# Kernel tuning notes

Hardware: AMD Instinct MI355X
Metric: run time of the kernel (lower is better)

The kernel has to match this reference:

```python
import jax, jax.numpy as jnp
import numpy as np

N, T, D, H = 64, 1024, 1024, 1024


def setup_inputs() -> dict:
    key = jax.random.key(0)
    k1, k2, k3, k4 = jax.random.split(key, 4)
    x = jax.random.normal(k1, (N, T, D), dtype=jnp.float32)
    h0 = jax.random.normal(k2, (N, H), dtype=jnp.float32)
    Wx = jax.random.normal(k3, (D, 4 * H), dtype=jnp.float32) / np.sqrt(D)
    Wh = jax.random.normal(k4, (H, 4 * H), dtype=jnp.float32) / np.sqrt(H)
    b = jnp.zeros((4 * H,), dtype=jnp.float32)
    return {"x": x, "h0": h0, "Wx": Wx, "Wh": Wh, "b": b}


def reference(x, h0, Wx, Wh, b):
    # x: [N, T, D], h0: [N, H] -> hn: [N, T, H]
    Hd = h0.shape[1]
    c0 = jnp.zeros_like(h0)
    # Precompute input contribution for all timesteps in one big GEMM:
    # identical math to per-step x_t @ Wx, far fewer launches.
    xW = jnp.einsum("ntd,dg->ntg", x, Wx) + b  # [N, T, 4H]

    def step(carry, xw_t):
        prev_h, prev_c = carry
        preact = xw_t + prev_h @ Wh  # [N, 4H]
        ai, af, ao, ag = jnp.split(preact, 4, axis=1)
        i = jax.nn.sigmoid(ai)
        f = jax.nn.sigmoid(af)
        o = jax.nn.sigmoid(ao)
        g = jnp.tanh(ag)
        next_c = f * prev_c + i * g
        next_h = o * jnp.tanh(next_c)
        return (next_h, next_c), next_h

    xW_t = jnp.swapaxes(xW, 0, 1)  # [T, N, 4H] for scan over time
    _, hs = jax.lax.scan(step, (h0, c0), xW_t)
    return jnp.swapaxes(hs, 0, 1)  # [N, T, H]
```

## Files before the change

### kernel.cpp

```cpp
#include <hip/hip_runtime.h>

typedef unsigned short u16;
typedef unsigned long long u64;
typedef __attribute__((ext_vector_type(8))) short short8;
typedef __attribute__((ext_vector_type(4))) float f32x4;

#define DEVINL __device__ __forceinline__

constexpr int Nb = 64;
constexpr int Tt = 1024;
constexpr int Dd = 1024;
constexpr int Hh = 1024;
constexpr int NWG = 256;
constexpr int TPB = 256;
constexpr int TWG = 128;
constexpr int MS  = 32;

DEVINL u16 f2b(float f) {
  union { float f; unsigned u; } v; v.f = f;
  unsigned r = (v.u + 0x7fffu + ((v.u >> 16) & 1u)) >> 16;
  return (u16)r;
}
DEVINL float sigm(float x) { return 1.f / (1.f + __expf(-x)); }
DEVINL float tanhfast(float x) { float e = __expf(2.f * x); return 1.f - 2.f / (e + 1.f); }

DEVINL short8 ldh16(const u16* p) {
  u64 a = __hip_atomic_load((const u64*)p,       __ATOMIC_RELAXED, __HIP_MEMORY_SCOPE_AGENT);
  u64 b = __hip_atomic_load((const u64*)(p + 4), __ATOMIC_RELAXED, __HIP_MEMORY_SCOPE_AGENT);
  union { u64 q[2]; short8 v; } u;
  u.q[0] = a; u.q[1] = b;
  return u.v;
}

DEVINL void bar_w() {
  asm volatile("s_waitcnt lgkmcnt(0)" ::: "memory");
  __builtin_amdgcn_s_barrier();
}

__global__ void cvt_x_kernel(const float* __restrict__ x, u16* __restrict__ xb) {
  size_t i = ((size_t)blockIdx.x * TPB + threadIdx.x) * 8;
  float4 a = *reinterpret_cast<const float4*>(x + i);
  float4 b = *reinterpret_cast<const float4*>(x + i + 4);
  short8 r;
  r[0] = (short)f2b(a.x); r[1] = (short)f2b(a.y);
  r[2] = (short)f2b(a.z); r[3] = (short)f2b(a.w);
  r[4] = (short)f2b(b.x); r[5] = (short)f2b(b.y);
  r[6] = (short)f2b(b.z); r[7] = (short)f2b(b.w);
  *reinterpret_cast<short8*>(xb + i) = r;
}

template<bool XBF16, bool HIST>
__global__ __launch_bounds__(TPB, 1) void lstm_team(
    const float* __restrict__ x, const u16* __restrict__ xb,
    const float* __restrict__ h0, const float* __restrict__ Wx,
    const float* __restrict__ Wh, const float* __restrict__ bias,
    float* __restrict__ out, u16* __restrict__ hmem,
    unsigned* __restrict__ flg)
{
  __shared__ u16 Bt[32][2048];
  __shared__ float ex[4][32][36];
  __shared__ unsigned pubcnt;

  const int g   = blockIdx.x;
  const int tid = threadIdx.x;
  const int w   = tid >> 6;
  const int l   = tid & 63;

  const int team = ((g & 7) < 4) ? 0 : 1;
  const int r    = (g >> 3) * 4 + (g & 3);
  const int n0   = team * MS;
  const int jc0  = r * 8;

  unsigned* tFlg = flg + team * TWG;
  u16* hb0 = HIST ? hmem + (size_t)team * ((size_t)Tt * MS * Hh)
                  : hmem + (size_t)team * (2 * MS * Hh);

  if (tid == 0) pubcnt = 0u;

  for (int idx = tid; idx < 32 * 2048; idx += TPB) {
    int k = idx >> 5;
    int c = idx & 31;
    int pc = (c >> 3) * 1024 + jc0 + (c & 7);
    float v = (k < 1024) ? Wh[(size_t)k * 4096 + pc]
                         : Wx[(size_t)(k - 1024) * 4096 + pc];
    Bt[c][k ^ ((c & 7) << 3)] = f2b(v);
  }

  if (tid < 64) {
    int n  = tid >> 1;
    int jc = (tid & 1) * 4;
    const float* hp = h0 + (size_t)(n0 + n) * Hh + jc0 + jc;
    u64 pk = (u64)f2b(hp[0]) | ((u64)f2b(hp[1]) << 16) |
             ((u64)f2b(hp[2]) << 32) | ((u64)f2b(hp[3]) << 48);
    __hip_atomic_store((u64*)(hb0 + n * Hh + jc0 + jc), pk,
                       __ATOMIC_RELAXED, __HIP_MEMORY_SCOPE_AGENT);
    asm volatile("s_waitcnt vmcnt(0)" ::: "memory");
    if (tid == 0)
      __hip_atomic_store(&tFlg[r], 1u, __ATOMIC_RELAXED, __HIP_MEMORY_SCOPE_AGENT);
  }
  __syncthreads();

  const int jj = tid & 7;
  const int nE = tid >> 3;
  const float bI = bias[0 * 1024 + jc0 + jj];
  const float bF = bias[1 * 1024 + jc0 + jj];
  const float bO = bias[2 * 1024 + jc0 + jj];
  const float bG = bias[3 * 1024 + jc0 + jj];
  float c_reg = 0.f;

  const int arow = l & 15;
  const int kg   = (l >> 4) * 8;
  const int kb   = w * 256;
  const int sw   = (l & 7) << 3;
  const u16* bp0 = &Bt[l & 15][0];
  const u16* bp1 = &Bt[16 | (l & 15)][0];

  short8 bh0[8], bh1[8], bx0[8], bx1[8];
  #pragma unroll
  for (int i = 0; i < 8; ++i) {
    int ka = (kb + kg + 32 * i) ^ sw;
    bh0[i] = *reinterpret_cast<const short8*>(bp0 + ka);
    bh1[i] = *reinterpret_cast<const short8*>(bp1 + ka);
    int kx = (1024 + kb + kg + 32 * i) ^ sw;
    bx0[i] = *reinterpret_cast<const short8*>(bp0 + kx);
    bx1[i] = *reinterpret_cast<const short8*>(bp1 + kx);
  }

  for (int t = 0; t < Tt; ++t) {
    const u16* hb  = HIST ? hb0 + (size_t)t * (MS * Hh)
                          : hb0 + (t & 1) * (MS * Hh);
    u16*       hbn = HIST ? hb0 + (size_t)(t + 1) * (MS * Hh)
                          : hb0 + ((t + 1) & 1) * (MS * Hh);

    short8 xv0[8], xv1[8];
    if constexpr (XBF16) {
      const u16* xr0 = xb + ((size_t)(n0 + arow)      * Tt + t) * Dd + kb + kg;
      const u16* xr1 = xb + ((size_t)(n0 + 16 + arow) * Tt + t) * Dd + kb + kg;
      #pragma unroll
      for (int i = 0; i < 8; ++i) {
        xv0[i] = *reinterpret_cast<const short8*>(xr0 + 32 * i);
        xv1[i] = *reinterpret_cast<const short8*>(xr1 + 32 * i);
      }
    } else {
      const float* xr0 = x + ((size_t)(n0 + arow)      * Tt + t) * Dd + kb + kg;
      const float* xr1 = x + ((size_t)(n0 + 16 + arow) * Tt + t) * Dd + kb + kg;
      #pragma unroll
      for (int i = 0; i < 8; ++i) {
        float4 a0 = *reinterpret_cast<const float4*>(xr0 + 32 * i);
        float4 a1 = *reinterpret_cast<const float4*>(xr0 + 32 * i + 4);
        float4 c0 = *reinterpret_cast<const float4*>(xr1 + 32 * i);
        float4 c1 = *reinterpret_cast<const float4*>(xr1 + 32 * i + 4);
        short8 v0, v1;
        v0[0]=(short)f2b(a0.x); v0[1]=(short)f2b(a0.y);
        v0[2]=(short)f2b(a0.z); v0[3]=(short)f2b(a0.w);
        v0[4]=(short)f2b(a1.x); v0[5]=(short)f2b(a1.y);
        v0[6]=(short)f2b(a1.z); v0[7]=(short)f2b(a1.w);
        v1[0]=(short)f2b(c0.x); v1[1]=(short)f2b(c0.y);
        v1[2]=(short)f2b(c0.z); v1[3]=(short)f2b(c0.w);
        v1[4]=(short)f2b(c1.x); v1[5]=(short)f2b(c1.y);
        v1[6]=(short)f2b(c1.z); v1[7]=(short)f2b(c1.w);
        xv0[i] = v0; xv1[i] = v1;
      }
    }

    f32x4 a00 = {0.f,0.f,0.f,0.f}, a01 = {0.f,0.f,0.f,0.f};
    f32x4 a10 = {0.f,0.f,0.f,0.f}, a11 = {0.f,0.f,0.f,0.f};

    #pragma unroll
    for (int i = 0; i < 8; ++i) {
      a00 = __builtin_amdgcn_mfma_f32_16x16x32_bf16(xv0[i], bx0[i], a00, 0, 0, 0);
      a01 = __builtin_amdgcn_mfma_f32_16x16x32_bf16(xv0[i], bx1[i], a01, 0, 0, 0);
      a10 = __builtin_amdgcn_mfma_f32_16x16x32_bf16(xv1[i], bx0[i], a10, 0, 0, 0);
      a11 = __builtin_amdgcn_mfma_f32_16x16x32_bf16(xv1[i], bx1[i], a11, 0, 0, 0);
    }

    {
      const unsigned ep = (unsigned)(t + 1);
      bool rdy;
      do {
        unsigned f = 0xFFFFFFFFu;
        if (l < 32)
          f = __hip_atomic_load(&tFlg[32 * w + l], __ATOMIC_RELAXED,
                                __HIP_MEMORY_SCOPE_AGENT);
        rdy = (bool)__all(f >= ep);
        if (!rdy) __builtin_amdgcn_s_sleep(1);
      } while (!rdy);
    }
    while (__hip_atomic_load(&pubcnt, __ATOMIC_RELAXED,
                             __HIP_MEMORY_SCOPE_WORKGROUP) < (unsigned)(4 * t))
      __builtin_amdgcn_s_sleep(1);
    asm volatile("" ::: "memory");

    short8 hv0[8], hv1[8];
    {
      const u16* hr = hb + (size_t)arow * Hh + kb + kg;
      #pragma unroll
      for (int i = 0; i < 8; ++i) {
        if constexpr (HIST) {
          hv0[i] = *reinterpret_cast<const short8*>(hr + 32 * i);
          hv1[i] = *reinterpret_cast<const short8*>(hr + 16 * Hh + 32 * i);
        } else {
          hv0[i] = ldh16(hr + 32 * i);
          hv1[i] = ldh16(hr + 16 * Hh + 32 * i);
        }
      }
    }

    #pragma unroll
    for (int i = 0; i < 8; ++i) {
      a00 = __builtin_amdgcn_mfma_f32_16x16x32_bf16(hv0[i], bh0[i], a00, 0, 0, 0);
      a01 = __builtin_amdgcn_mfma_f32_16x16x32_bf16(hv0[i], bh1[i], a01, 0, 0, 0);
      a10 = __builtin_amdgcn_mfma_f32_16x16x32_bf16(hv1[i], bh0[i], a10, 0, 0, 0);
      a11 = __builtin_amdgcn_mfma_f32_16x16x32_bf16(hv1[i], bh1[i], a11, 0, 0, 0);
    }

    #pragma unroll
    for (int q = 0; q < 4; ++q) {
      ex[w][ 0 + (l >> 4) * 4 + q][ 0 + (l & 15)] = a00[q];
      ex[w][ 0 + (l >> 4) * 4 + q][16 + (l & 15)] = a01[q];
      ex[w][16 + (l >> 4) * 4 + q][ 0 + (l & 15)] = a10[q];
      ex[w][16 + (l >> 4) * 4 + q][16 + (l & 15)] = a11[q];
    }
    bar_w();

    float pI = bI, pF = bF, pO = bO, pG = bG;
    #pragma unroll
    for (int wv = 0; wv < 4; ++wv) {
      pI += ex[wv][nE][ 0 + jj];
      pF += ex[wv][nE][ 8 + jj];
      pO += ex[wv][nE][16 + jj];
      pG += ex[wv][nE][24 + jj];
    }
    const float ig = sigm(pI), fg = sigm(pF), og = sigm(pO);
    const float gg = tanhfast(pG);
    c_reg = fg * c_reg + ig * gg;
    const float hv = og * tanhfast(c_reg);

    {
      int hb16 = (int)f2b(hv);
      int pb   = __shfl_xor(hb16, 1, 64);
      if ((tid & 1) == 0) {
        unsigned pk = (unsigned)(hb16 & 0xFFFF) | ((unsigned)(pb & 0xFFFF) << 16);
        __hip_atomic_store((unsigned*)(hbn + nE * Hh + jc0 + jj), pk,
                           __ATOMIC_RELAXED, __HIP_MEMORY_SCOPE_AGENT);
      }
      asm volatile("s_waitcnt vmcnt(0)" ::: "memory");
      if (l == 0) {
        unsigned old = __hip_atomic_fetch_add(&pubcnt, 1u, __ATOMIC_RELAXED,
                                              __HIP_MEMORY_SCOPE_WORKGROUP);
        if (old == (unsigned)(4 * t + 3) && t + 1 < Tt)
          __hip_atomic_store(&tFlg[r], (unsigned)(t + 2),
                             __ATOMIC_RELAXED, __HIP_MEMORY_SCOPE_AGENT);
      }
    }

    out[((size_t)(n0 + nE) * Tt + t) * Hh + jc0 + jj] = hv;
  }
}

extern "C" void kernel_launch(void* const* d_in, const int* in_sizes, int n_in,
                              void* d_out, int out_size, void* d_ws, size_t ws_size,
                              hipStream_t stream) {
  const float* x    = (const float*)d_in[0];
  const float* h0   = (const float*)d_in[1];
  const float* Wx   = (const float*)d_in[2];
  const float* Wh   = (const float*)d_in[3];
  const float* bias = (const float*)d_in[4];
  float* out = (float*)d_out;

  char* wsb = (char*)d_ws;
  unsigned* flg = (unsigned*)wsb;

  const size_t hist_off   = (size_t)1 << 20;
  const size_t hist_bytes = (size_t)2 * Tt * MS * Hh * 2;
  const size_t xb_bytes   = (size_t)Nb * Tt * Dd * 2;

  const bool use_hist = ws_size >= hist_off + hist_bytes;
  const size_t xb_off = use_hist ? hist_off + hist_bytes : hist_off;
  const bool use_xb   = ws_size >= xb_off + xb_bytes;

  u16* hmem = use_hist ? (u16*)(wsb + hist_off) : (u16*)(wsb + 65536);
  u16* xb   = (u16*)(wsb + xb_off);

  hipMemsetAsync(wsb, 0, 40960, stream);

  void* args[] = {(void*)&x, (void*)&xb, (void*)&h0, (void*)&Wx, (void*)&Wh,
                  (void*)&bias, (void*)&out, (void*)&hmem, (void*)&flg};
  if (use_xb)
    cvt_x_kernel<<<dim3((Nb * Tt * Dd) / (8 * TPB)), dim3(TPB), 0, stream>>>(x, xb);

  const void* kfn =
      use_hist ? (use_xb ? (const void*)lstm_team<true, true>
                         : (const void*)lstm_team<false, true>)
               : (use_xb ? (const void*)lstm_team<true, false>
                         : (const void*)lstm_team<false, false>);
  hipLaunchCooperativeKernel(kfn, dim3(NWG), dim3(TPB), args, 0, stream);
}
```

Baseline: 5.635 ms.

## Precompute input projection with a separate bf16 MFMA GEMM before recurrent kernel

Adds a transposed bf16 conversion of Wx and a tiled, double-buffered MFMA GEMM that computes x@Wx for all timesteps into workspace, in fp32 or bf16 depending on workspace size. The persistent LSTM kernel then loads the precomputed gate preactivations instead of running the x-side MFMAs each step, which shortens the serial per-step critical path. In exchange it writes and reads a large intermediate (up to 1 GiB fp32) and runs extra kernels. It falls back to the old fused path when workspace is too small.

```diff
diff --git a/kernel.cpp b/kernel.cpp
--- a/kernel.cpp
+++ b/kernel.cpp
@@ -20,6 +20,10 @@
   union { float f; unsigned u; } v; v.f = f;
   unsigned r = (v.u + 0x7fffu + ((v.u >> 16) & 1u)) >> 16;
   return (u16)r;
+}
+DEVINL float b2f(u16 b) {
+  union { unsigned u; float f; } v; v.u = ((unsigned)b) << 16;
+  return v.f;
 }
 DEVINL float sigm(float x) { return 1.f / (1.f + __expf(-x)); }
 DEVINL float tanhfast(float x) { float e = __expf(2.f * x); return 1.f - 2.f / (e + 1.f); }
@@ -49,13 +53,105 @@
   *reinterpret_cast<short8*>(xb + i) = r;
 }
 
-template<bool XBF16, bool HIST>
+__global__ void cvt_wt_kernel(const float* __restrict__ wx, u16* __restrict__ wxt) {
+  int gid = blockIdx.x * TPB + threadIdx.x;
+  int k  = gid >> 9;
+  int nb = (gid & 511) * 8;
+  const float* p = wx + (size_t)k * 4096 + nb;
+  #pragma unroll
+  for (int i = 0; i < 8; ++i)
+    wxt[(size_t)(nb + i) * 1024 + k] = f2b(p[i]);
+}
+
+template<bool F32OUT>
+__global__ __launch_bounds__(TPB) void gemm_xw(
+    const u16* __restrict__ A, const u16* __restrict__ B, void* __restrict__ C)
+{
+  __shared__ u16 Al[2][128][40];
+  __shared__ u16 Bl[2][128][40];
+  const int tid = threadIdx.x;
+  const int w = tid >> 6, l = tid & 63;
+  const int mt = blockIdx.x >> 5, nt = blockIdx.x & 31;
+  const size_t m0 = (size_t)mt * 128, n0 = (size_t)nt * 128;
+  const int wr = w >> 1, wc = w & 1;
+  const int srow = tid >> 2;
+  const int scol = (tid & 3) * 8;
+  const int arow = l & 15, kg = (l >> 4) * 8;
+
+  f32x4 acc[4][4];
+  #pragma unroll
+  for (int i = 0; i < 4; ++i)
+    #pragma unroll
+    for (int j = 0; j < 4; ++j) acc[i][j] = (f32x4){0.f, 0.f, 0.f, 0.f};
+
+  #pragma unroll
+  for (int rr = 0; rr < 2; ++rr) {
+    int row = rr * 64 + srow;
+    short8 sa = *reinterpret_cast<const short8*>(A + (m0 + row) * 1024 + scol);
+    short8 sb = *reinterpret_cast<const short8*>(B + (n0 + row) * 1024 + scol);
+    *reinterpret_cast<short8*>(&Al[0][row][scol]) = sa;
+    *reinterpret_cast<short8*>(&Bl[0][row][scol]) = sb;
+  }
+  bar_w();
+
+  int cur = 0;
+  for (int ks = 0; ks < 32; ++ks) {
+    short8 na[2], nb2[2];
+    if (ks < 31) {
+      #pragma unroll
+      for (int rr = 0; rr < 2; ++rr) {
+        int row = rr * 64 + srow;
+        na[rr]  = *reinterpret_cast<const short8*>(A + (m0 + row) * 1024 + (ks + 1) * 32 + scol);
+        nb2[rr] = *reinterpret_cast<const short8*>(B + (n0 + row) * 1024 + (ks + 1) * 32 + scol);
+      }
+    }
+    short8 av[4], bv[4];
+    #pragma unroll
+    for (int tr = 0; tr < 4; ++tr)
+      av[tr] = *reinterpret_cast<const short8*>(&Al[cur][wr * 64 + tr * 16 + arow][kg]);
+    #pragma unroll
+    for (int tc = 0; tc < 4; ++tc)
+      bv[tc] = *reinterpret_cast<const short8*>(&Bl[cur][wc * 64 + tc * 16 + arow][kg]);
+    #pragma unroll
+    for (int tr = 0; tr < 4; ++tr)
+      #pragma unroll
+      for (int tc = 0; tc < 4; ++tc)
+        acc[tr][tc] = __builtin_amdgcn_mfma_f32_16x16x32_bf16(av[tr], bv[tc], acc[tr][tc], 0, 0, 0);
+    if (ks < 31) {
+      #pragma unroll
+      for (int rr = 0; rr < 2; ++rr) {
+        int row = rr * 64 + srow;
+        *reinterpret_cast<short8*>(&Al[cur ^ 1][row][scol]) = na[rr];
+        *reinterpret_cast<short8*>(&Bl[cur ^ 1][row][scol]) = nb2[rr];
+      }
+    }
+    bar_w();
+    cur ^= 1;
+  }
+
+  #pragma unroll
+  for (int tr = 0; tr < 4; ++tr) {
+    int mrow = wr * 64 + tr * 16 + 4 * (l >> 4);
+    #pragma unroll
+    for (int tc = 0; tc < 4; ++tc) {
+      int ncol = wc * 64 + tc * 16 + (l & 15);
+      #pragma unroll
+      for (int q = 0; q < 4; ++q) {
+        size_t off = (m0 + mrow + q) * 4096 + n0 + ncol;
+        if constexpr (F32OUT) ((float*)C)[off] = acc[tr][tc][q];
+        else                  ((u16*)C)[off]   = f2b(acc[tr][tc][q]);
+      }
+    }
+  }
+}
+
+template<int MODE, bool XBF16, bool HIST>
 __global__ __launch_bounds__(TPB, 1) void lstm_team(
     const float* __restrict__ x, const u16* __restrict__ xb,
     const float* __restrict__ h0, const float* __restrict__ Wx,
     const float* __restrict__ Wh, const float* __restrict__ bias,
     float* __restrict__ out, u16* __restrict__ hmem,
-    unsigned* __restrict__ flg)
+    unsigned* __restrict__ flg, const void* __restrict__ xw)
 {
   __shared__ u16 Bt[32][2048];
   __shared__ float ex[4][32][36];
@@ -77,12 +173,16 @@
 
   if (tid == 0) pubcnt = 0u;
 
-  for (int idx = tid; idx < 32 * 2048; idx += TPB) {
-    int k = idx >> 5;
+  constexpr int KW = (MODE == 0) ? 2048 : 1024;
+  for (int idx = tid; idx < 32 * KW; idx += TPB) {
+    int k = idx / 32;
     int c = idx & 31;
     int pc = (c >> 3) * 1024 + jc0 + (c & 7);
-    float v = (k < 1024) ? Wh[(size_t)k * 4096 + pc]
-                         : Wx[(size_t)(k - 1024) * 4096 + pc];
+    float v;
+    if constexpr (MODE == 0)
+      v = (k < 1024) ? Wh[(size_t)k * 4096 + pc] : Wx[(size_t)(k - 1024) * 4096 + pc];
+    else
+      v = Wh[(size_t)k * 4096 + pc];
     Bt[c][k ^ ((c & 7) << 3)] = f2b(v);
   }
 
@@ -121,57 +221,65 @@
     int ka = (kb + kg + 32 * i) ^ sw;
     bh0[i] = *reinterpret_cast<const short8*>(bp0 + ka);
     bh1[i] = *reinterpret_cast<const short8*>(bp1 + ka);
-    int kx = (1024 + kb + kg + 32 * i) ^ sw;
-    bx0[i] = *reinterpret_cast<const short8*>(bp0 + kx);
-    bx1[i] = *reinterpret_cast<const short8*>(bp1 + kx);
+    if constexpr (MODE == 0) {
+      int kx = (1024 + kb + kg + 32 * i) ^ sw;
+      bx0[i] = *reinterpret_cast<const short8*>(bp0 + kx);
+      bx1[i] = *reinterpret_cast<const short8*>(bp1 + kx);
+    }
   }
 
   for (int t = 0; t < Tt; ++t) {
-    const u16* hb  = HIST ? hb0 + (size_t)t * (MS * Hh)
-                          : hb0 + (t & 1) * (MS * Hh);
-    u16*       hbn = HIST ? hb0 + (size_t)(t + 1) * (MS * Hh)
-                          : hb0 + ((t + 1) & 1) * (MS * Hh);
-
-    short8 xv0[8], xv1[8];
-    if constexpr (XBF16) {
-      const u16* xr0 = xb + ((size_t)(n0 + arow)      * Tt + t) * Dd + kb + kg;
-      const u16* xr1 = xb + ((size_t)(n0 + 16 + arow) * Tt + t) * Dd + kb + kg;
-      #pragma unroll
-      for (int i = 0; i < 8; ++i) {
-        xv0[i] = *reinterpret_cast<const short8*>(xr0 + 32 * i);
-        xv1[i] = *reinterpret_cast<const short8*>(xr1 + 32 * i);
-      }
-    } else {
-      const float* xr0 = x + ((size_t)(n0 + arow)      * Tt + t) * Dd + kb + kg;
-      const float* xr1 = x + ((size_t)(n0 + 16 + arow) * Tt + t) * Dd + kb + kg;
-      #pragma unroll
-      for (int i = 0; i < 8; ++i) {
-        float4 a0 = *reinterpret_cast<const float4*>(xr0 + 32 * i);
-        float4 a1 = *reinterpret_cast<const float4*>(xr0 + 32 * i + 4);
-        float4 c0 = *reinterpret_cast<const float4*>(xr1 + 32 * i);
-        float4 c1 = *reinterpret_cast<const float4*>(xr1 + 32 * i + 4);
-        short8 v0, v1;
-        v0[0]=(short)f2b(a0.x); v0[1]=(short)f2b(a0.y);
-        v0[2]=(short)f2b(a0.z); v0[3]=(short)f2b(a0.w);
-        v0[4]=(short)f2b(a1.x); v0[5]=(short)f2b(a1.y);
-        v0[6]=(short)f2b(a1.z); v0[7]=(short)f2b(a1.w);
-        v1[0]=(short)f2b(c0.x); v1[1]=(short)f2b(c0.y);
-        v1[2]=(short)f2b(c0.z); v1[3]=(short)f2b(c0.w);
-        v1[4]=(short)f2b(c1.x); v1[5]=(short)f2b(c1.y);
-        v1[6]=(short)f2b(c1.z); v1[7]=(short)f2b(c1.w);
-        xv0[i] = v0; xv1[i] = v1;
-      }
-    }
+    const u16* hb  = HIST ? hb0 + (size_t)t * (MS * Hh) : hb0 + (t & 1) * (MS * Hh);
+    u16*       hbn = HIST ? hb0 + (size_t)(t + 1) * (MS * Hh) : hb0 + ((t + 1) & 1) * (MS * Hh);
 
     f32x4 a00 = {0.f,0.f,0.f,0.f}, a01 = {0.f,0.f,0.f,0.f};
     f32x4 a10 = {0.f,0.f,0.f,0.f}, a11 = {0.f,0.f,0.f,0.f};
-
-    #pragma unroll
-    for (int i = 0; i < 8; ++i) {
-      a00 = __builtin_amdgcn_mfma_f32_16x16x32_bf16(xv0[i], bx0[i], a00, 0, 0, 0);
-      a01 = __builtin_amdgcn_mfma_f32_16x16x32_bf16(xv0[i], bx1[i], a01, 0, 0, 0);
-      a10 = __builtin_amdgcn_mfma_f32_16x16x32_bf16(xv1[i], bx0[i], a10, 0, 0, 0);
-      a11 = __builtin_amdgcn_mfma_f32_16x16x32_bf16(xv1[i], bx1[i], a11, 0, 0, 0);
+    float xwv0 = 0.f, xwv1 = 0.f, xwv2 = 0.f, xwv3 = 0.f;
+
+    if constexpr (MODE == 0) {
+      short8 xv0[8], xv1[8];
+      if constexpr (XBF16) {
+        const u16* xr0 = xb + ((size_t)(n0 + arow)      * Tt + t) * Dd + kb + kg;
+        const u16* xr1 = xb + ((size_t)(n0 + 16 + arow) * Tt + t) * Dd + kb + kg;
+        #pragma unroll
+        for (int i = 0; i < 8; ++i) {
+          xv0[i] = *reinterpret_cast<const short8*>(xr0 + 32 * i);
+          xv1[i] = *reinterpret_cast<const short8*>(xr1 + 32 * i);
+        }
+      } else {
+        const float* xr0 = x + ((size_t)(n0 + arow)      * Tt + t) * Dd + kb + kg;
+        const float* xr1 = x + ((size_t)(n0 + 16 + arow) * Tt + t) * Dd + kb + kg;
+        #pragma unroll
+        for (int i = 0; i < 8; ++i) {
+          float4 a0 = *reinterpret_cast<const float4*>(xr0 + 32 * i);
+          float4 a1 = *reinterpret_cast<const float4*>(xr0 + 32 * i + 4);
+          float4 c0 = *reinterpret_cast<const float4*>(xr1 + 32 * i);
+          float4 c1 = *reinterpret_cast<const float4*>(xr1 + 32 * i + 4);
+          short8 v0, v1;
+          v0[0]=(short)f2b(a0.x); v0[1]=(short)f2b(a0.y);
+          v0[2]=(short)f2b(a0.z); v0[3]=(short)f2b(a0.w);
+          v0[4]=(short)f2b(a1.x); v0[5]=(short)f2b(a1.y);
+          v0[6]=(short)f2b(a1.z); v0[7]=(short)f2b(a1.w);
+          v1[0]=(short)f2b(c0.x); v1[1]=(short)f2b(c0.y);
+          v1[2]=(short)f2b(c0.z); v1[3]=(short)f2b(c0.w);
+          v1[4]=(short)f2b(c1.x); v1[5]=(short)f2b(c1.y);
+          v1[6]=(short)f2b(c1.z); v1[7]=(short)f2b(c1.w);
+          xv0[i] = v0; xv1[i] = v1;
+        }
+      }
+      #pragma unroll
+      for (int i = 0; i < 8; ++i) {
+        a00 = __builtin_amdgcn_mfma_f32_16x16x32_bf16(xv0[i], bx0[i], a00, 0, 0, 0);
+        a01 = __builtin_amdgcn_mfma_f32_16x16x32_bf16(xv0[i], bx1[i], a01, 0, 0, 0);
+        a10 = __builtin_amdgcn_mfma_f32_16x16x32_bf16(xv1[i], bx0[i], a10, 0, 0, 0);
+        a11 = __builtin_amdgcn_mfma_f32_16x16x32_bf16(xv1[i], bx1[i], a11, 0, 0, 0);
+      }
+    } else if constexpr (MODE == 1) {
+      const float* p = (const float*)xw + ((size_t)(n0 + nE) * Tt + t) * 4096 + jc0 + jj;
+      xwv0 = p[0]; xwv1 = p[1024]; xwv2 = p[2048]; xwv3 = p[3072];
+    } else {
+      const u16* p = (const u16*)xw + ((size_t)(n0 + nE) * Tt + t) * 4096 + jc0 + jj;
+      xwv0 = b2f(p[0]); xwv1 = b2f(p[1024]); xwv2 = b2f(p[2048]); xwv3 = b2f(p[3072]);
     }
 
     {
@@ -223,7 +331,7 @@
     }
     bar_w();
 
-    float pI = bI, pF = bF, pO = bO, pG = bG;
+    float pI = bI + xwv0, pF = bF + xwv1, pO = bO + xwv2, pG = bG + xwv3;
     #pragma unroll
     for (int wv = 0; wv < 4; ++wv) {
       pI += ex[wv][nE][ 0 + jj];
@@ -271,28 +379,60 @@
   char* wsb = (char*)d_ws;
   unsigned* flg = (unsigned*)wsb;
 
-  const size_t hist_off   = (size_t)1 << 20;
-  const size_t hist_bytes = (size_t)2 * Tt * MS * Hh * 2;
-  const size_t xb_bytes   = (size_t)Nb * Tt * Dd * 2;
-
-  const bool use_hist = ws_size >= hist_off + hist_bytes;
-  const size_t xb_off = use_hist ? hist_off + hist_bytes : hist_off;
-  const bool use_xb   = ws_size >= xb_off + xb_bytes;
-
-  u16* hmem = use_hist ? (u16*)(wsb + hist_off) : (u16*)(wsb + 65536);
-  u16* xb   = (u16*)(wsb + xb_off);
+  const size_t off_hist = (size_t)1 << 20;
+  const size_t sz_hist  = (size_t)2 * Tt * MS * Hh * 2;
+  const size_t off_xb   = off_hist + sz_hist;
+  const size_t sz_xb    = (size_t)Nb * Tt * Dd * 2;
+  const size_t off_wt   = off_xb + sz_xb;
+  const size_t sz_wt    = (size_t)4096 * 1024 * 2;
+  const size_t off_xw   = off_wt + sz_wt;
+  const size_t sz_xw32  = (size_t)Nb * Tt * 4096 * 4;
+  const size_t sz_xw16  = sz_xw32 / 2;
+
+  int mode;
+  if      (ws_size >= off_xw + sz_xw32) mode = 1;
+  else if (ws_size >= off_xw + sz_xw16) mode = 2;
+  else                                  mode = 0;
+
+  u16* hmem;
+  u16* xb  = (u16*)(wsb + off_xb);
+  u16* wxt = (u16*)(wsb + off_wt);
+  void* xw = (void*)(wsb + off_xw);
 
   hipMemsetAsync(wsb, 0, 40960, stream);
 
-  void* args[] = {(void*)&x, (void*)&xb, (void*)&h0, (void*)&Wx, (void*)&Wh,
-                  (void*)&bias, (void*)&out, (void*)&hmem, (void*)&flg};
+  if (mode >= 1) {
+    hmem = (u16*)(wsb + off_hist);
+    cvt_x_kernel<<<dim3((Nb * Tt * Dd) / (8 * TPB)), dim3(TPB), 0, stream>>>(x, xb);
+    cvt_wt_kernel<<<dim3(2048), dim3(TPB), 0, stream>>>(Wx, wxt);
+    if (mode == 1)
+      gemm_xw<true><<<dim3(16384), dim3(TPB), 0, stream>>>(xb, wxt, xw);
+    else
+      gemm_xw<false><<<dim3(16384), dim3(TPB), 0, stream>>>(xb, wxt, xw);
+
+    void* args[] = {(void*)&x, (void*)&xb, (void*)&h0, (void*)&Wx, (void*)&Wh,
+                    (void*)&bias, (void*)&out, (void*)&hmem, (void*)&flg, (void*)&xw};
+    const void* kfn = (mode == 1) ? (const void*)lstm_team<1, false, true>
+                                  : (const void*)lstm_team<2, false, true>;
+    hipLaunchCooperativeKernel(kfn, dim3(NWG), dim3(TPB), args, 0, stream);
+    return;
+  }
+
+  const bool use_hist = ws_size >= off_hist + sz_hist;
+  const size_t xb0_off = use_hist ? off_xb : off_hist;
+  const bool use_xb   = ws_size >= xb0_off + sz_xb;
+  hmem = use_hist ? (u16*)(wsb + off_hist) : (u16*)(wsb + 65536);
+  u16* xb0 = (u16*)(wsb + xb0_off);
+
+  void* args[] = {(void*)&x, (void*)&xb0, (void*)&h0, (void*)&Wx, (void*)&Wh,
+                  (void*)&bias, (void*)&out, (void*)&hmem, (void*)&flg, (void*)&xw};
   if (use_xb)
-    cvt_x_kernel<<<dim3((Nb * Tt * Dd) / (8 * TPB)), dim3(TPB), 0, stream>>>(x, xb);
+    cvt_x_kernel<<<dim3((Nb * Tt * Dd) / (8 * TPB)), dim3(TPB), 0, stream>>>(x, xb0);
 
   const void* kfn =
-      use_hist ? (use_xb ? (const void*)lstm_team<true, true>
-                         : (const void*)lstm_team<false, true>)
-               : (use_xb ? (const void*)lstm_team<true, false>
-                         : (const void*)lstm_team<false, false>);
+      use_hist ? (use_xb ? (const void*)lstm_team<0, true,  true>
+                         : (const void*)lstm_team<0, false, true>)
+               : (use_xb ? (const void*)lstm_team<0, true,  false>
+                         : (const void*)lstm_team<0, false, false>);
   hipLaunchCooperativeKernel(kfn, dim3(NWG), dim3(TPB), args, 0, stream);
 }
```

New measurement: 8.155 ms. +44.7%, slower.
